# Performance work log

Measured on AMD Instinct MI355X. Metric: run time of the kernel, lower is better.

Reference implementation:

```python
import jax, jax.numpy as jnp
import numpy as np

HEAD_DIM = 64
SCALE = HEAD_DIM ** (-0.5)


def setup_inputs() -> dict:
    key = jax.random.key(0)
    kq, kk, kv = jax.random.split(key, 3)
    B, H, S, D = 2, 12, 2048, HEAD_DIM
    query = jax.random.normal(kq, (B, H, S, D), dtype=jnp.float32)
    k = jax.random.normal(kk, (B, H, S, D), dtype=jnp.float32)
    v = jax.random.normal(kv, (B, H, S, D), dtype=jnp.float32)
    mask = jnp.ones((1, 1, S, S), dtype=jnp.int32)
    return {"query": query, "key": k, "value": v, "mask": mask}


def reference(query, key, value, mask):
    # scores: [B, H, S, S]
    scores = jnp.einsum("bhqd,bhkd->bhqk", query, key) * SCALE
    scores = jnp.where(mask == 0, -jnp.inf, scores)
    probs = jax.nn.softmax(scores, axis=-1)
    # dropout = 0.0 -> identity
    out = jnp.einsum("bhqk,bhkd->bhqd", probs, value)
    return out
```

## Files before the change

### kernel.cpp

```cpp
#include <hip/hip_runtime.h>

#define SDIM 2048
#define DDIM 64
#define NT   32
#define SCL2  (0.125f * 1.4426950408889634f)

typedef __attribute__((ext_vector_type(8))) short          bf16x8;
typedef __attribute__((ext_vector_type(8))) unsigned short ushort8;
typedef __attribute__((ext_vector_type(4))) float          f32x4;
typedef __attribute__((ext_vector_type(16))) float         f32x16;

__device__ __forceinline__ unsigned short f2bf(float x) {
    unsigned int u = __float_as_uint(x);
    u += 0x7FFFu + ((u >> 16) & 1u);
    return (unsigned short)(u >> 16);
}

__device__ __forceinline__ void cp16(const void* g, void* l) {
    __builtin_amdgcn_global_load_lds(
        (__attribute__((address_space(1))) void*)(uintptr_t)g,
        (__attribute__((address_space(3))) void*)(unsigned int)(uintptr_t)l,
        16, 0, 0);
}

__global__ __launch_bounds__(256)
void prep_kv(const float* __restrict__ Kp, const float* __restrict__ Vp,
             unsigned short* __restrict__ wsK, unsigned short* __restrict__ wsV)
{
    __shared__ alignas(16) unsigned short vstage[64 * DDIM];
    const int tid = threadIdx.x;
    const int t   = blockIdx.x;
    const int bh  = blockIdx.y;
    const size_t tb   = ((size_t)bh * NT + t) * (64 * DDIM);
    const size_t gsrc = (size_t)bh * SDIM * DDIM + (size_t)t * 64 * DDIM;

    const int key = tid >> 2;
    const int d0  = (tid & 3) << 4;
    const int sw  = (key & 7) << 3;

    {
        const float* src = Kp + gsrc + key * DDIM + d0;
        float4 a0 = ((const float4*)src)[0];
        float4 a1 = ((const float4*)src)[1];
        float4 a2 = ((const float4*)src)[2];
        float4 a3 = ((const float4*)src)[3];
        ushort8 w0, w1;
        w0[0]=f2bf(a0.x); w0[1]=f2bf(a0.y); w0[2]=f2bf(a0.z); w0[3]=f2bf(a0.w);
        w0[4]=f2bf(a1.x); w0[5]=f2bf(a1.y); w0[6]=f2bf(a1.z); w0[7]=f2bf(a1.w);
        w1[0]=f2bf(a2.x); w1[1]=f2bf(a2.y); w1[2]=f2bf(a2.z); w1[3]=f2bf(a2.w);
        w1[4]=f2bf(a3.x); w1[5]=f2bf(a3.y); w1[6]=f2bf(a3.z); w1[7]=f2bf(a3.w);
        *(ushort8*)&wsK[tb + key * 64 + ( d0      ^ sw)] = w0;
        *(ushort8*)&wsK[tb + key * 64 + ((d0 + 8) ^ sw)] = w1;
    }
    {
        const float* src = Vp + gsrc + key * DDIM + d0;
        float4 a0 = ((const float4*)src)[0];
        float4 a1 = ((const float4*)src)[1];
        float4 a2 = ((const float4*)src)[2];
        float4 a3 = ((const float4*)src)[3];
        ushort8 w0, w1;
        w0[0]=f2bf(a0.x); w0[1]=f2bf(a0.y); w0[2]=f2bf(a0.z); w0[3]=f2bf(a0.w);
        w0[4]=f2bf(a1.x); w0[5]=f2bf(a1.y); w0[6]=f2bf(a1.z); w0[7]=f2bf(a1.w);
        w1[0]=f2bf(a2.x); w1[1]=f2bf(a2.y); w1[2]=f2bf(a2.z); w1[3]=f2bf(a2.w);
        w1[4]=f2bf(a3.x); w1[5]=f2bf(a3.y); w1[6]=f2bf(a3.z); w1[7]=f2bf(a3.w);
        *(ushort8*)&vstage[key * 64 + ( d0      ^ sw)] = w0;
        *(ushort8*)&vstage[key * 64 + ((d0 + 8) ^ sw)] = w1;
    }
    __syncthreads();
    {
        const int d   = tid >> 2;
        const int k0  = (tid & 3) << 4;
        const int st  = k0 >> 5;
        const int kh  = (k0 >> 4) & 1;
        const int dsw = (d >> 1) & 3;
        unsigned short vals[16];
        #pragma unroll
        for (int m = 0; m < 16; ++m) {
            const int k = k0 + m;
            vals[m] = vstage[k * 64 + (d ^ ((k & 7) << 3))];
        }
        const size_t vbase = tb + st * 2048 + d * 32;
        #pragma unroll
        for (int hh = 0; hh < 2; ++hh) {
            ushort8 o;
            #pragma unroll
            for (int j = 0; j < 8; ++j)
                o[j] = vals[(j & 3) + 4 * hh + 8 * (j >> 2)];
            *(ushort8*)&wsV[vbase + (((2 * kh + hh) ^ dsw) << 3)] = o;
        }
    }
}

__global__ __launch_bounds__(256, 3)
void attn64_main(const float* __restrict__ Qp,
                 const unsigned short* __restrict__ wsK,
                 const unsigned short* __restrict__ wsV,
                 float* __restrict__ Op, int bhpx)
{
    __shared__ alignas(16) unsigned short kbuf[6][2048];
    __shared__ alignas(16) unsigned short vbuf[6][2048];

    const int tid  = threadIdx.x;
    const int lane = tid & 63;
    const int w    = tid >> 6;
    const int qh   = w & 1;
    const int par  = w >> 1;
    const int l5   = lane & 31;
    const int h    = lane >> 5;

    const int blk = blockIdx.x;
    int bh, qt;
    if (bhpx) {
        const int loc = blk >> 3;
        bh = (blk & 7) * bhpx + (loc >> 5);
        qt = loc & 31;
    } else {
        bh = blk >> 5;
        qt = blk & 31;
    }

    const unsigned short* Kt = wsK + (size_t)bh * (SDIM * DDIM);
    const unsigned short* Vt = wsV + (size_t)bh * (SDIM * DDIM);

    const unsigned short* gK = Kt + tid * 8;
    const unsigned short* gV = Vt + tid * 8;

    auto stagepair = [&](int p, int SN) {
        const unsigned short* gk = gK + (size_t)p * 4096;
        const unsigned short* gv = gV + (size_t)p * 4096;
        cp16(gk,        &kbuf[SN][tid * 8]);
        cp16(gk + 2048, &kbuf[SN + 1][tid * 8]);
        cp16(gv,        &vbuf[SN][tid * 8]);
        cp16(gv + 2048, &vbuf[SN + 1][tid * 8]);
    };

    stagepair(0, 0);
    stagepair(1, 2);

    bf16x8 qf[4];
    {
        const float* Qb = Qp + (size_t)bh * SDIM * DDIM;
        const int qrow = qt * 64 + qh * 32 + l5;
        #pragma unroll
        for (int ks = 0; ks < 4; ++ks) {
            const float* src = Qb + (size_t)qrow * DDIM + ks * 16 + h * 8;
            float4 a = ((const float4*)src)[0];
            float4 b = ((const float4*)src)[1];
            bf16x8 tq;
            tq[0] = (short)f2bf(a.x * SCL2); tq[1] = (short)f2bf(a.y * SCL2);
            tq[2] = (short)f2bf(a.z * SCL2); tq[3] = (short)f2bf(a.w * SCL2);
            tq[4] = (short)f2bf(b.x * SCL2); tq[5] = (short)f2bf(b.y * SCL2);
            tq[6] = (short)f2bf(b.z * SCL2); tq[7] = (short)f2bf(b.w * SCL2);
            qf[ks] = tq;
        }
    }

    int kaddr[4];
    #pragma unroll
    for (int ks = 0; ks < 4; ++ks)
        kaddr[ks] = l5 * 64 + ((ks * 16 + h * 8) ^ ((l5 & 7) << 3));
    int vaddr[2][2];
    #pragma unroll
    for (int kh = 0; kh < 2; ++kh)
        #pragma unroll
        for (int dh = 0; dh < 2; ++dh) {
            const int d = dh * 32 + l5;
            vaddr[kh][dh] = d * 32 + (((2 * kh + h) ^ ((d >> 1) & 3)) << 3);
        }

    const short ov = (l5 == 0) ? (short)0x3F80 : (short)0;
    const bf16x8 af = { ov, ov, ov, ov, ov, ov, ov, ov };

    f32x16 oacc0, oacc1, acc5;
    #pragma unroll
    for (int i = 0; i < 16; ++i) { oacc0[i] = 0.f; oacc1[i] = 0.f; acc5[i] = 0.f; }

    auto tilebody = [&](const unsigned short* kb, const unsigned short* vb) {
        f32x16 s;
        #pragma unroll
        for (int i = 0; i < 16; ++i) s[i] = 0.f;
        __builtin_amdgcn_s_setprio(1);
        #pragma unroll
        for (int ks = 0; ks < 4; ++ks) {
            bf16x8 kf = *(const bf16x8*)&kb[kaddr[ks]];
            s = __builtin_amdgcn_mfma_f32_32x32x16_bf16(kf, qf[ks], s, 0, 0, 0);
        }
        __builtin_amdgcn_s_setprio(0);
        union { unsigned int u[8]; bf16x8 v[2]; } P;
        #pragma unroll
        for (int i = 0; i < 8; ++i) {
            const float p0 = exp2f(s[2 * i]);
            const float p1 = exp2f(s[2 * i + 1]);
            unsigned int r;
            asm("v_cvt_pk_bf16_f32 %0, %1, %2" : "=v"(r) : "v"(p0), "v"(p1));
            P.u[i] = r;
        }
        __builtin_amdgcn_s_setprio(1);
        acc5 = __builtin_amdgcn_mfma_f32_32x32x16_bf16(af, P.v[0], acc5, 0, 0, 0);
        {
            bf16x8 v00 = *(const bf16x8*)&vb[vaddr[0][0]];
            oacc0 = __builtin_amdgcn_mfma_f32_32x32x16_bf16(v00, P.v[0], oacc0, 0, 0, 0);
            bf16x8 v01 = *(const bf16x8*)&vb[vaddr[0][1]];
            oacc1 = __builtin_amdgcn_mfma_f32_32x32x16_bf16(v01, P.v[0], oacc1, 0, 0, 0);
        }
        acc5 = __builtin_amdgcn_mfma_f32_32x32x16_bf16(af, P.v[1], acc5, 0, 0, 0);
        {
            bf16x8 v10 = *(const bf16x8*)&vb[vaddr[1][0]];
            oacc0 = __builtin_amdgcn_mfma_f32_32x32x16_bf16(v10, P.v[1], oacc0, 0, 0, 0);
            bf16x8 v11 = *(const bf16x8*)&vb[vaddr[1][1]];
            oacc1 = __builtin_amdgcn_mfma_f32_32x32x16_bf16(v11, P.v[1], oacc1, 0, 0, 0);
        }
        __builtin_amdgcn_s_setprio(0);
    };

    asm volatile("s_waitcnt vmcnt(4) lgkmcnt(0)" ::: "memory");
    __builtin_amdgcn_s_barrier();

    int pcur = 0;
    auto pairstep = [&](int SC, int SN, bool do_stage, bool last) {
        if (do_stage) stagepair(pcur + 2, SN);
        tilebody(&kbuf[SC + par][0], &vbuf[SC + par][0]);
        if (do_stage) { asm volatile("s_waitcnt vmcnt(4) lgkmcnt(0)" ::: "memory"); }
        else          { asm volatile("s_waitcnt vmcnt(0) lgkmcnt(0)" ::: "memory"); }
        if (!last) __builtin_amdgcn_s_barrier();
        ++pcur;
    };

    #pragma unroll 1
    for (int jj = 0; jj < 10; ++jj) {
        pairstep(0, 4, true, false);
        pairstep(2, 0, true, false);
        pairstep(4, 2, true, false);
    }
    pairstep(0, 4, false, false);
    pairstep(2, 0, false, true);

    __syncthreads();
    float* comb = (float*)&kbuf[0][0];
    const int cb = (qh * 64 + lane) * 36;
    if (par) {
        #pragma unroll
        for (int g = 0; g < 4; ++g) {
            f32x4 t0 = { oacc0[4*g], oacc0[4*g+1], oacc0[4*g+2], oacc0[4*g+3] };
            *(f32x4*)&comb[cb + 4 * g] = t0;
            f32x4 t1 = { oacc1[4*g], oacc1[4*g+1], oacc1[4*g+2], oacc1[4*g+3] };
            *(f32x4*)&comb[cb + 16 + 4 * g] = t1;
        }
        comb[cb + 32] = acc5[0];
    }
    __syncthreads();
    if (!par) {
        #pragma unroll
        for (int g = 0; g < 4; ++g) {
            f32x4 t0 = *(const f32x4*)&comb[cb + 4 * g];
            oacc0[4*g] += t0[0]; oacc0[4*g+1] += t0[1]; oacc0[4*g+2] += t0[2]; oacc0[4*g+3] += t0[3];
            f32x4 t1 = *(const f32x4*)&comb[cb + 16 + 4 * g];
            oacc1[4*g] += t1[0]; oacc1[4*g+1] += t1[1]; oacc1[4*g+2] += t1[2]; oacc1[4*g+3] += t1[3];
        }
        const float ls0  = acc5[0] + comb[cb + 32];
        const float lsum = __shfl(ls0, l5);
        const float inv  = 1.f / lsum;
        const int q = qt * 64 + qh * 32 + l5;
        float* dst = Op + (size_t)bh * SDIM * DDIM + (size_t)q * DDIM;
        #pragma unroll
        for (int rg = 0; rg < 4; ++rg) {
            float4 o0 = { oacc0[4*rg] * inv, oacc0[4*rg+1] * inv,
                          oacc0[4*rg+2] * inv, oacc0[4*rg+3] * inv };
            *(float4*)&dst[8 * rg + 4 * h] = o0;
            float4 o1 = { oacc1[4*rg] * inv, oacc1[4*rg+1] * inv,
                          oacc1[4*rg+2] * inv, oacc1[4*rg+3] * inv };
            *(float4*)&dst[32 + 8 * rg + 4 * h] = o1;
        }
    }
}

typedef __attribute__((ext_vector_type(4))) short bf16x4;

__global__ __launch_bounds__(256)
void attn64_fallback(const float* __restrict__ Qp, const float* __restrict__ Kp,
                     const float* __restrict__ Vp, float* __restrict__ Op)
{
    __shared__ alignas(16) unsigned short kls[64 * DDIM];
    __shared__ alignas(16) unsigned short vls[DDIM * 64];
    __shared__ alignas(16) unsigned short pls[4][16 * 64];

    const int tid  = threadIdx.x;
    const int lane = tid & 63;
    const int wave = tid >> 6;
    const int lo4  = lane & 15;
    const int hi2  = lane >> 4;
    const int qt = blockIdx.x;
    const int bh = blockIdx.y;

    const size_t base = (size_t)bh * SDIM * DDIM;
    const float* Qb = Qp + base;
    const float* Kb = Kp + base;
    const float* Vb = Vp + base;
    float*       Ob = Op + base;

    bf16x8 qf[2];
    {
        const int qrow = qt * 64 + wave * 16 + lo4;
        #pragma unroll
        for (int ks = 0; ks < 2; ++ks) {
            const float* src = Qb + (size_t)qrow * DDIM + ks * 32 + hi2 * 8;
            float4 a = ((const float4*)src)[0];
            float4 b = ((const float4*)src)[1];
            bf16x8 tq;
            tq[0] = (short)f2bf(a.x * SCL2); tq[1] = (short)f2bf(a.y * SCL2);
            tq[2] = (short)f2bf(a.z * SCL2); tq[3] = (short)f2bf(a.w * SCL2);
            tq[4] = (short)f2bf(b.x * SCL2); tq[5] = (short)f2bf(b.y * SCL2);
            tq[6] = (short)f2bf(b.z * SCL2); tq[7] = (short)f2bf(b.w * SCL2);
            qf[ks] = tq;
        }
    }

    float mrow[4], lrow[4];
    f32x4 oacc[4];
    #pragma unroll
    for (int r = 0; r < 4; ++r) { mrow[r] = -1e30f; lrow[r] = 0.f; }
    #pragma unroll
    for (int n = 0; n < 4; ++n) oacc[n] = f32x4{0.f, 0.f, 0.f, 0.f};

    for (int t0 = 0; t0 < SDIM; t0 += 64) {
        __syncthreads();
        {
            const int key = tid >> 2;
            const int d0  = (tid & 3) << 4;
            const float* src = Kb + (size_t)(t0 + key) * DDIM + d0;
            float4 a0 = ((const float4*)src)[0];
            float4 a1 = ((const float4*)src)[1];
            float4 a2 = ((const float4*)src)[2];
            float4 a3 = ((const float4*)src)[3];
            ushort8 w0, w1;
            w0[0]=f2bf(a0.x); w0[1]=f2bf(a0.y); w0[2]=f2bf(a0.z); w0[3]=f2bf(a0.w);
            w0[4]=f2bf(a1.x); w0[5]=f2bf(a1.y); w0[6]=f2bf(a1.z); w0[7]=f2bf(a1.w);
            w1[0]=f2bf(a2.x); w1[1]=f2bf(a2.y); w1[2]=f2bf(a2.z); w1[3]=f2bf(a2.w);
            w1[4]=f2bf(a3.x); w1[5]=f2bf(a3.y); w1[6]=f2bf(a3.z); w1[7]=f2bf(a3.w);
            const int sw = (key & 7) << 3;
            *(ushort8*)&kls[key * 64 + ( d0      ^ sw)] = w0;
            *(ushort8*)&kls[key * 64 + ((d0 + 8) ^ sw)] = w1;
        }
        {
            const int key = lane;
            const int d0  = wave << 4;
            const float* src = Vb + (size_t)(t0 + key) * DDIM + d0;
            float4 b0 = ((const float4*)src)[0];
            float4 b1 = ((const float4*)src)[1];
            float4 b2 = ((const float4*)src)[2];
            float4 b3 = ((const float4*)src)[3];
            float vv[16] = { b0.x,b0.y,b0.z,b0.w, b1.x,b1.y,b1.z,b1.w,
                             b2.x,b2.y,b2.z,b2.w, b3.x,b3.y,b3.z,b3.w };
            #pragma unroll
            for (int j = 0; j < 16; ++j) {
                const int d = d0 + j;
                vls[d * 64 + (key ^ ((d & 7) << 3))] = f2bf(vv[j]);
            }
        }
        __syncthreads();

        f32x4 s[4];
        #pragma unroll
        for (int n = 0; n < 4; ++n) s[n] = f32x4{0.f, 0.f, 0.f, 0.f};
        #pragma unroll
        for (int ks = 0; ks < 2; ++ks) {
            const int kb = ks * 32 + hi2 * 8;
            #pragma unroll
            for (int n = 0; n < 4; ++n) {
                const int key = lo4 + 16 * n;
                bf16x8 b = *(const bf16x8*)&kls[key * 64 + (kb ^ ((key & 7) << 3))];
                s[n] = __builtin_amdgcn_mfma_f32_16x16x32_bf16(qf[ks], b, s[n], 0, 0, 0);
            }
        }
        #pragma unroll
        for (int r = 0; r < 4; ++r) {
            float tmax = fmaxf(fmaxf(s[0][r], s[1][r]), fmaxf(s[2][r], s[3][r]));
            tmax = fmaxf(tmax, __shfl_xor(tmax, 1));
            tmax = fmaxf(tmax, __shfl_xor(tmax, 2));
            tmax = fmaxf(tmax, __shfl_xor(tmax, 4));
            tmax = fmaxf(tmax, __shfl_xor(tmax, 8));
            const float mn   = fmaxf(mrow[r], tmax);
            const float corr = exp2f(mrow[r] - mn);
            mrow[r] = mn;
            float rs = 0.f;
            #pragma unroll
            for (int n = 0; n < 4; ++n) {
                const float p = exp2f(s[n][r] - mn);
                s[n][r] = p;
                rs += p;
            }
            rs += __shfl_xor(rs, 1);
            rs += __shfl_xor(rs, 2);
            rs += __shfl_xor(rs, 4);
            rs += __shfl_xor(rs, 8);
            lrow[r] = lrow[r] * corr + rs;
            #pragma unroll
            for (int n = 0; n < 4; ++n) oacc[n][r] *= corr;
        }
        #pragma unroll
        for (int r = 0; r < 4; ++r) {
            const int q  = hi2 * 4 + r;
            const int sw = (q & 7) << 3;
            #pragma unroll
            for (int n = 0; n < 4; ++n)
                pls[wave][q * 64 + ((lo4 + 16 * n) ^ sw)] = f2bf(s[n][r]);
        }
        __syncthreads();
        #pragma unroll
        for (int ks = 0; ks < 2; ++ks) {
            const int kb = ks * 32 + hi2 * 8;
            bf16x8 a = *(const bf16x8*)&pls[wave][lo4 * 64 + (kb ^ ((lo4 & 7) << 3))];
            #pragma unroll
            for (int n = 0; n < 4; ++n) {
                const int d = 16 * n + lo4;
                bf16x8 b = *(const bf16x8*)&vls[d * 64 + (kb ^ ((d & 7) << 3))];
                oacc[n] = __builtin_amdgcn_mfma_f32_16x16x32_bf16(a, b, oacc[n], 0, 0, 0);
            }
        }
    }
    #pragma unroll
    for (int r = 0; r < 4; ++r) {
        const float inv = 1.f / lrow[r];
        const int q = qt * 64 + wave * 16 + hi2 * 4 + r;
        float* dst = Ob + (size_t)q * DDIM;
        #pragma unroll
        for (int n = 0; n < 4; ++n)
            dst[16 * n + lo4] = oacc[n][r] * inv;
    }
}

extern "C" void kernel_launch(void* const* d_in, const int* in_sizes, int n_in,
                              void* d_out, int out_size, void* d_ws, size_t ws_size,
                              hipStream_t stream) {
    const float* Q = (const float*)d_in[0];
    const float* K = (const float*)d_in[1];
    const float* V = (const float*)d_in[2];
    float* O = (float*)d_out;
    const int BH = in_sizes[0] / (SDIM * DDIM);
    const size_t need = 2ull * BH * SDIM * DDIM * sizeof(unsigned short);

    if (ws_size >= need) {
        unsigned short* wsK = (unsigned short*)d_ws;
        unsigned short* wsV = wsK + (size_t)BH * SDIM * DDIM;
        const int bhpx = (BH % 8 == 0) ? (BH / 8) : 0;
        prep_kv<<<dim3(NT, BH), dim3(256), 0, stream>>>(K, V, wsK, wsV);
        attn64_main<<<dim3(BH * 32), dim3(256), 0, stream>>>(Q, wsK, wsV, O, bhpx);
    } else {
        attn64_fallback<<<dim3(SDIM / 64, BH), dim3(256), 0, stream>>>(Q, K, V, O);
    }
}
```

Baseline: 55.30 us.

## Load K/V tiles directly from global into registers, dropping LDS staging

Removes the LDS triple-buffered global_load_lds pipeline and its per-tile barriers. Each wave now reads pre-swizzled K/V fragments straight from global memory into registers, prefetching the next K tile one iteration ahead. The row sum of P is now accumulated on the VALU instead of through an extra ones-vector MFMA. With far less LDS in use, the occupancy hint rises from 3 to 4 blocks per CU. The trade-off is that every wave issues its own global/L2 loads with no cross-wave sharing, and V loads are not prefetched, so their latency is exposed inside the loop.

```diff
diff --git a/kernel.cpp b/kernel.cpp
--- a/kernel.cpp
+++ b/kernel.cpp
@@ -14,13 +14,6 @@
     unsigned int u = __float_as_uint(x);
     u += 0x7FFFu + ((u >> 16) & 1u);
     return (unsigned short)(u >> 16);
-}
-
-__device__ __forceinline__ void cp16(const void* g, void* l) {
-    __builtin_amdgcn_global_load_lds(
-        (__attribute__((address_space(1))) void*)(uintptr_t)g,
-        (__attribute__((address_space(3))) void*)(unsigned int)(uintptr_t)l,
-        16, 0, 0);
 }
 
 __global__ __launch_bounds__(256)
@@ -91,14 +84,13 @@
     }
 }
 
-__global__ __launch_bounds__(256, 3)
+__global__ __launch_bounds__(256, 4)
 void attn64_main(const float* __restrict__ Qp,
                  const unsigned short* __restrict__ wsK,
                  const unsigned short* __restrict__ wsV,
                  float* __restrict__ Op, int bhpx)
 {
-    __shared__ alignas(16) unsigned short kbuf[6][2048];
-    __shared__ alignas(16) unsigned short vbuf[6][2048];
+    __shared__ float comb[2 * 64 * 33];
 
     const int tid  = threadIdx.x;
     const int lane = tid & 63;
@@ -121,21 +113,6 @@
 
     const unsigned short* Kt = wsK + (size_t)bh * (SDIM * DDIM);
     const unsigned short* Vt = wsV + (size_t)bh * (SDIM * DDIM);
-
-    const unsigned short* gK = Kt + tid * 8;
-    const unsigned short* gV = Vt + tid * 8;
-
-    auto stagepair = [&](int p, int SN) {
-        const unsigned short* gk = gK + (size_t)p * 4096;
-        const unsigned short* gv = gV + (size_t)p * 4096;
-        cp16(gk,        &kbuf[SN][tid * 8]);
-        cp16(gk + 2048, &kbuf[SN + 1][tid * 8]);
-        cp16(gv,        &vbuf[SN][tid * 8]);
-        cp16(gv + 2048, &vbuf[SN + 1][tid * 8]);
-    };
-
-    stagepair(0, 0);
-    stagepair(1, 2);
 
     bf16x8 qf[4];
     {
@@ -168,24 +145,40 @@
             vaddr[kh][dh] = d * 32 + (((2 * kh + h) ^ ((d >> 1) & 3)) << 3);
         }
 
-    const short ov = (l5 == 0) ? (short)0x3F80 : (short)0;
-    const bf16x8 af = { ov, ov, ov, ov, ov, ov, ov, ov };
-
-    f32x16 oacc0, oacc1, acc5;
-    #pragma unroll
-    for (int i = 0; i < 16; ++i) { oacc0[i] = 0.f; oacc1[i] = 0.f; acc5[i] = 0.f; }
-
-    auto tilebody = [&](const unsigned short* kb, const unsigned short* vb) {
+    f32x16 oacc0, oacc1;
+    #pragma unroll
+    for (int i = 0; i < 16; ++i) { oacc0[i] = 0.f; oacc1[i] = 0.f; }
+    float rs = 0.f;
+
+    const unsigned short* kp = Kt + par * 2048;
+    const unsigned short* vp = Vt + par * 2048;
+
+    bf16x8 kf[4];
+    #pragma unroll
+    for (int ks = 0; ks < 4; ++ks) kf[ks] = *(const bf16x8*)&kp[kaddr[ks]];
+
+    #pragma unroll 1
+    for (int it = 0; it < 32; ++it) {
         f32x16 s;
         #pragma unroll
         for (int i = 0; i < 16; ++i) s[i] = 0.f;
         __builtin_amdgcn_s_setprio(1);
         #pragma unroll
-        for (int ks = 0; ks < 4; ++ks) {
-            bf16x8 kf = *(const bf16x8*)&kb[kaddr[ks]];
-            s = __builtin_amdgcn_mfma_f32_32x32x16_bf16(kf, qf[ks], s, 0, 0, 0);
-        }
+        for (int ks = 0; ks < 4; ++ks)
+            s = __builtin_amdgcn_mfma_f32_32x32x16_bf16(kf[ks], qf[ks], s, 0, 0, 0);
         __builtin_amdgcn_s_setprio(0);
+
+        bf16x8 v00 = *(const bf16x8*)&vp[vaddr[0][0]];
+        bf16x8 v01 = *(const bf16x8*)&vp[vaddr[0][1]];
+        bf16x8 v10 = *(const bf16x8*)&vp[vaddr[1][0]];
+        bf16x8 v11 = *(const bf16x8*)&vp[vaddr[1][1]];
+
+        kp += 4096;
+        if (it < 31) {
+            #pragma unroll
+            for (int ks = 0; ks < 4; ++ks) kf[ks] = *(const bf16x8*)&kp[kaddr[ks]];
+        }
+
         union { unsigned int u[8]; bf16x8 v[2]; } P;
         #pragma unroll
         for (int i = 0; i < 8; ++i) {
@@ -194,59 +187,30 @@
             unsigned int r;
             asm("v_cvt_pk_bf16_f32 %0, %1, %2" : "=v"(r) : "v"(p0), "v"(p1));
             P.u[i] = r;
-        }
+            rs += __uint_as_float(r << 16) + __uint_as_float(r & 0xFFFF0000u);
+        }
+
         __builtin_amdgcn_s_setprio(1);
-        acc5 = __builtin_amdgcn_mfma_f32_32x32x16_bf16(af, P.v[0], acc5, 0, 0, 0);
-        {
-            bf16x8 v00 = *(const bf16x8*)&vb[vaddr[0][0]];
-            oacc0 = __builtin_amdgcn_mfma_f32_32x32x16_bf16(v00, P.v[0], oacc0, 0, 0, 0);
-            bf16x8 v01 = *(const bf16x8*)&vb[vaddr[0][1]];
-            oacc1 = __builtin_amdgcn_mfma_f32_32x32x16_bf16(v01, P.v[0], oacc1, 0, 0, 0);
-        }
-        acc5 = __builtin_amdgcn_mfma_f32_32x32x16_bf16(af, P.v[1], acc5, 0, 0, 0);
-        {
-            bf16x8 v10 = *(const bf16x8*)&vb[vaddr[1][0]];
-            oacc0 = __builtin_amdgcn_mfma_f32_32x32x16_bf16(v10, P.v[1], oacc0, 0, 0, 0);
-            bf16x8 v11 = *(const bf16x8*)&vb[vaddr[1][1]];
-            oacc1 = __builtin_amdgcn_mfma_f32_32x32x16_bf16(v11, P.v[1], oacc1, 0, 0, 0);
-        }
+        oacc0 = __builtin_amdgcn_mfma_f32_32x32x16_bf16(v00, P.v[0], oacc0, 0, 0, 0);
+        oacc1 = __builtin_amdgcn_mfma_f32_32x32x16_bf16(v01, P.v[0], oacc1, 0, 0, 0);
+        oacc0 = __builtin_amdgcn_mfma_f32_32x32x16_bf16(v10, P.v[1], oacc0, 0, 0, 0);
+        oacc1 = __builtin_amdgcn_mfma_f32_32x32x16_bf16(v11, P.v[1], oacc1, 0, 0, 0);
         __builtin_amdgcn_s_setprio(0);
-    };
-
-    asm volatile("s_waitcnt vmcnt(4) lgkmcnt(0)" ::: "memory");
-    __builtin_amdgcn_s_barrier();
-
-    int pcur = 0;
-    auto pairstep = [&](int SC, int SN, bool do_stage, bool last) {
-        if (do_stage) stagepair(pcur + 2, SN);
-        tilebody(&kbuf[SC + par][0], &vbuf[SC + par][0]);
-        if (do_stage) { asm volatile("s_waitcnt vmcnt(4) lgkmcnt(0)" ::: "memory"); }
-        else          { asm volatile("s_waitcnt vmcnt(0) lgkmcnt(0)" ::: "memory"); }
-        if (!last) __builtin_amdgcn_s_barrier();
-        ++pcur;
-    };
-
-    #pragma unroll 1
-    for (int jj = 0; jj < 10; ++jj) {
-        pairstep(0, 4, true, false);
-        pairstep(2, 0, true, false);
-        pairstep(4, 2, true, false);
-    }
-    pairstep(0, 4, false, false);
-    pairstep(2, 0, false, true);
+
+        vp += 4096;
+    }
+
+    rs += __shfl_xor(rs, 32);
 
     __syncthreads();
-    float* comb = (float*)&kbuf[0][0];
-    const int cb = (qh * 64 + lane) * 36;
+    const int cb = (qh * 64 + lane) * 33;
     if (par) {
         #pragma unroll
         for (int g = 0; g < 4; ++g) {
-            f32x4 t0 = { oacc0[4*g], oacc0[4*g+1], oacc0[4*g+2], oacc0[4*g+3] };
-            *(f32x4*)&comb[cb + 4 * g] = t0;
-            f32x4 t1 = { oacc1[4*g], oacc1[4*g+1], oacc1[4*g+2], oacc1[4*g+3] };
-            *(f32x4*)&comb[cb + 16 + 4 * g] = t1;
-        }
-        comb[cb + 32] = acc5[0];
+            *(f32x4*)&comb[cb + 4 * g]      = f32x4{ oacc0[4*g], oacc0[4*g+1], oacc0[4*g+2], oacc0[4*g+3] };
+            *(f32x4*)&comb[cb + 16 + 4 * g] = f32x4{ oacc1[4*g], oacc1[4*g+1], oacc1[4*g+2], oacc1[4*g+3] };
+        }
+        comb[cb + 32] = rs;
     }
     __syncthreads();
     if (!par) {
@@ -257,8 +221,7 @@
             f32x4 t1 = *(const f32x4*)&comb[cb + 16 + 4 * g];
             oacc1[4*g] += t1[0]; oacc1[4*g+1] += t1[1]; oacc1[4*g+2] += t1[2]; oacc1[4*g+3] += t1[3];
         }
-        const float ls0  = acc5[0] + comb[cb + 32];
-        const float lsum = __shfl(ls0, l5);
+        const float lsum = rs + comb[cb + 32];
         const float inv  = 1.f / lsum;
         const int q = qt * 64 + qh * 32 + l5;
         float* dst = Op + (size_t)bh * SDIM * DDIM + (size_t)q * DDIM;
```

After: 58.28 us. 1.05x slower.
